# Optimization experiments

Measured on AMD Instinct MI355X. Metric: run time of the kernel, lower is better.

The kernel has to match this reference:

```python
import jax, jax.numpy as jnp
import numpy as np

# static config (matches init_kwargs)
B, CIN, L = 32, 128, 4096
COUT, K = 256, 5
PAD_SIZE = 2
INPUT_SCALE = 0.05
OUTPUT_SCALE = 0.1
INPUT_ZP = -3
OUTPUT_ZP = -128
QMIN, QMAX = -128, 127  # 8-bit signed range


def setup_inputs() -> dict:
    key = jax.random.key(0)
    k1, k2, k3, k4 = jax.random.split(key, 4)
    x = jax.random.normal(k1, (B, CIN, L), dtype=jnp.float32)
    weight = jax.random.randint(k2, (COUT, CIN, K), -127, 128, dtype=jnp.int32).astype(jnp.int8)
    # shifted quantized bias (int32), plausible magnitude
    bias = jax.random.randint(k3, (COUT,), -20000, 20000, dtype=jnp.int32)
    # per-output-channel weight scale
    weight_scale = jax.random.uniform(k4, (COUT,), dtype=jnp.float32, minval=1e-3, maxval=1e-2)
    return {"x": x, "weight": weight, "bias": bias, "weight_scale": weight_scale}


def reference(x, weight, bias, weight_scale):
    # --- linear_quantize (first_layer) ---
    xq = jnp.round(x / INPUT_SCALE) + INPUT_ZP
    xq = jnp.clip(xq, QMIN, QMAX).astype(jnp.int8)
    # --- ReplicationPad1d(pad_size) ---
    xq = jnp.pad(xq, ((0, 0), (0, 0), (PAD_SIZE, PAD_SIZE)), mode="edge")
    # --- int8 conv1d with int32 accumulation ---
    acc = jax.lax.conv_general_dilated(
        xq.astype(jnp.int32), weight.astype(jnp.int32),
        window_strides=(1,), padding=[(0, 0)],
        dimension_numbers=("NCH", "OIH", "NCH"))  # [B, COUT, Lout]
    acc = acc + bias[None, :, None]
    # --- per-channel requantization ---
    scale = (INPUT_SCALE * weight_scale / OUTPUT_SCALE)[None, :, None]
    out = acc.astype(jnp.float32) * scale + OUTPUT_ZP
    out = jnp.clip(jnp.round(out), QMIN, QMAX).astype(jnp.int8)
    return out
```

## Files before the change

### kernel.cpp

```cpp
#include <hip/hip_runtime.h>


#define B_    32
#define CIN   128
#define LEN   4096
#define COUT  256
#define KW    5
#define TROWS 136

#define WTF_BYTES (KW * 2 * 16 * 64 * 16)

typedef int          i32x4 __attribute__((ext_vector_type(4)));
typedef signed char  s8;

__device__ __forceinline__ s8 quant_i8(float xv) {
    float q = rintf(fmaf(xv, 20.0f, -3.0f));
    q = fminf(fmaxf(q, -128.0f), 127.0f);
    return (s8)(int)q;
}

__global__ __launch_bounds__(256) void wprep_kernel(
        const int* __restrict__ w, const int* __restrict__ bias,
        const float* __restrict__ wscale,
        s8* __restrict__ wtf, float* __restrict__ tbl)
{
    int o    = blockIdx.x * 256 + threadIdx.x;
    int lane = o & 63, frag = o >> 6;
    int k    = frag >> 5;
    int s    = (frag >> 4) & 1;
    int co   = ((frag & 15) << 4) + (lane & 15);
    int ci   = (s << 6) + ((lane >> 4) << 4);
    union { s8 c[16]; i32x4 v; } q;
    #pragma unroll
    for (int j = 0; j < 16; ++j)
        q.c[j] = (s8)w[co * (CIN * KW) + (ci + j) * KW + k];
    *(i32x4*)(wtf + (size_t)frag * 1024 + lane * 16) = q.v;

    if (blockIdx.x == 0) {
        int c = threadIdx.x;
        float sc = __fdiv_rn(__fmul_rn(0.05f, wscale[c]), 0.1f);
        tbl[c]       = sc;
        tbl[256 + c] = fmaf((float)bias[c], sc, -128.0f);
    }
}

__global__ __launch_bounds__(512, 4) void conv_fused(
        const float* __restrict__ x, const s8* __restrict__ wtf,
        const float* __restrict__ tbl, int* __restrict__ out)
{
    __shared__ __align__(16) s8 smem[TROWS * CIN];

    int orig  = (blockIdx.x & 7) * 128 + (blockIdx.x >> 3);
    int ltile = orig & 31;
    int b     = orig >> 5;
    int l0    = ltile << 7;
    int tid   = threadIdx.x;
    int wid   = tid >> 6, lane = tid & 63;
    int lr    = lane & 15, lh = lane >> 4;
    int cog   = (wid & 3) << 6;
    int wl    = (wid >> 2) << 6;

    const float* xb = x + (size_t)b * CIN * LEN;

    {
        const float* src = xb + (size_t)(wid << 4) * LEN;
        int gl0 = min(max(l0 - 4 + lane, 0), LEN - 1);
        int gl1 = min(max(l0 + 60 + lane, 0), LEN - 1);
        float v0[16], v1[16];
        #pragma unroll
        for (int j = 0; j < 16; ++j) {
            v0[j] = src[(size_t)j * LEN + gl0];
            v1[j] = src[(size_t)j * LEN + gl1];
        }
        union { s8 cc[16]; i32x4 v; } q0, q1;
        #pragma unroll
        for (int j = 0; j < 16; ++j) q0.cc[j] = quant_i8(v0[j]);
        #pragma unroll
        for (int j = 0; j < 16; ++j) q1.cc[j] = quant_i8(v1[j]);
        int row0 = lane, row1 = 64 + lane;
        *(i32x4*)(smem + (row0 << 7) + ((wid ^ (row0 & 7)) << 4)) = q0.v;
        *(i32x4*)(smem + (row1 << 7) + ((wid ^ (row1 & 7)) << 4)) = q1.v;
        if (lane < 8) {
            int row2 = 128 + lane;
            int gl2 = min(max(l0 + 124 + lane, 0), LEN - 1);
            union { s8 cc[16]; i32x4 v; } q2;
            #pragma unroll
            for (int j = 0; j < 16; ++j)
                q2.cc[j] = quant_i8(src[(size_t)j * LEN + gl2]);
            *(i32x4*)(smem + (row2 << 7) + ((wid ^ (row2 & 7)) << 4)) = q2.v;
        }
    }
    __syncthreads();

    i32x4 acc[4][4] = {};
    #pragma unroll
    for (int k = 0; k < KW; ++k) {
        #pragma unroll
        for (int s = 0; s < 2; ++s) {
            i32x4 af[4];
            #pragma unroll
            for (int ct = 0; ct < 4; ++ct)
                af[ct] = *(const i32x4*)(
                    wtf + (size_t)((k << 5) + (s << 4) + (cog >> 4) + ct) * 1024 + lane * 16);
            i32x4 bf[4];
            int chunk = (s << 2) + lh;
            #pragma unroll
            for (int lt = 0; lt < 4; ++lt) {
                int row = wl + (lt << 4) + lr + k + 2;
                bf[lt] = *(const i32x4*)(smem + (row << 7) + ((chunk ^ (row & 7)) << 4));
            }
            #pragma unroll
            for (int ct = 0; ct < 4; ++ct)
                #pragma unroll
                for (int lt = 0; lt < 4; ++lt)
                    acc[ct][lt] = __builtin_amdgcn_mfma_i32_16x16x64_i8(
                        bf[lt], af[ct], acc[ct][lt], 0, 0, 0);
        }
    }

    size_t outb = (size_t)b * COUT * LEN;
    #pragma unroll
    for (int ct = 0; ct < 4; ++ct) {
        int co = cog + (ct << 4) + lr;
        float scv = tbl[co];
        float off = tbl[256 + co];
        int* orow = out + outb + (size_t)co * LEN + l0 + wl + (lh << 2);
        #pragma unroll
        for (int lt = 0; lt < 4; ++lt) {
            i32x4 pk;
            #pragma unroll
            for (int r = 0; r < 4; ++r) {
                float o = rintf(fmaf((float)acc[ct][lt][r], scv, off));
                o = fminf(fmaxf(o, -128.0f), 127.0f);
                pk[r] = (int)o;
            }
            *(i32x4*)(orow + (lt << 4)) = pk;
        }
    }
}

extern "C" void kernel_launch(void* const* d_in, const int* in_sizes, int n_in,
                              void* d_out, int out_size, void* d_ws, size_t ws_size,
                              hipStream_t stream)
{
    const float* x    = (const float*)d_in[0];
    const int*   w    = (const int*)d_in[1];
    const int*   bias = (const int*)d_in[2];
    const float* wsc  = (const float*)d_in[3];
    int* out = (int*)d_out;

    s8*    wtf = (s8*)d_ws;
    float* tbl = (float*)((char*)d_ws + WTF_BYTES);

    wprep_kernel<<<dim3(40), dim3(256), 0, stream>>>(w, bias, wsc, wtf, tbl);
    conv_fused<<<dim3(1024), dim3(512), 0, stream>>>(x, wtf, tbl, out);
}
```

Before: 54.99 us.

## Halve conv tile length to 64 positions with 256-thread blocks

Each block now covers 64 output positions instead of 128, using 4 waves that each own 64 output channels, and the grid doubles to 2048 blocks. The input staging is reorganised so each wave loads two 16-channel groups, and the clamp on border indices is applied only for edge tiles. This gives more, smaller blocks and less shared memory per block, which should help occupancy and scheduling. The cost is a larger halo share per tile, so more redundant input loading and quantisation, and each weight fragment is reused across fewer positions.

```diff
diff --git a/kernel.cpp b/kernel.cpp
--- a/kernel.cpp
+++ b/kernel.cpp
@@ -6,7 +6,7 @@
 #define LEN   4096
 #define COUT  256
 #define KW    5
-#define TROWS 136
+#define TROWS 72
 
 #define WTF_BYTES (KW * 2 * 16 * 64 * 16)
 
@@ -44,50 +44,57 @@
     }
 }
 
-__global__ __launch_bounds__(512, 4) void conv_fused(
+__global__ __launch_bounds__(256, 4) void conv_fused(
         const float* __restrict__ x, const s8* __restrict__ wtf,
         const float* __restrict__ tbl, int* __restrict__ out)
 {
     __shared__ __align__(16) s8 smem[TROWS * CIN];
 
-    int orig  = (blockIdx.x & 7) * 128 + (blockIdx.x >> 3);
-    int ltile = orig & 31;
-    int b     = orig >> 5;
-    int l0    = ltile << 7;
+    int orig  = (blockIdx.x & 7) * 256 + (blockIdx.x >> 3);
+    int ltile = orig & 63;
+    int b     = orig >> 6;
+    int l0    = ltile << 6;
     int tid   = threadIdx.x;
     int wid   = tid >> 6, lane = tid & 63;
     int lr    = lane & 15, lh = lane >> 4;
-    int cog   = (wid & 3) << 6;
-    int wl    = (wid >> 2) << 6;
+    int cog   = wid << 6;
 
     const float* xb = x + (size_t)b * CIN * LEN;
 
     {
-        const float* src = xb + (size_t)(wid << 4) * LEN;
-        int gl0 = min(max(l0 - 4 + lane, 0), LEN - 1);
-        int gl1 = min(max(l0 + 60 + lane, 0), LEN - 1);
+        bool edge = (ltile == 0) | (ltile == 63);
+        const float* src0 = xb + (size_t)(wid << 4) * LEN;
+        const float* src1 = xb + (size_t)((wid + 4) << 4) * LEN;
+        int gl0 = l0 - 4 + lane;
+        if (edge) gl0 = min(max(gl0, 0), LEN - 1);
         float v0[16], v1[16];
         #pragma unroll
-        for (int j = 0; j < 16; ++j) {
-            v0[j] = src[(size_t)j * LEN + gl0];
-            v1[j] = src[(size_t)j * LEN + gl1];
-        }
+        for (int j = 0; j < 16; ++j) v0[j] = src0[(size_t)j * LEN + gl0];
+        #pragma unroll
+        for (int j = 0; j < 16; ++j) v1[j] = src1[(size_t)j * LEN + gl0];
         union { s8 cc[16]; i32x4 v; } q0, q1;
         #pragma unroll
         for (int j = 0; j < 16; ++j) q0.cc[j] = quant_i8(v0[j]);
         #pragma unroll
         for (int j = 0; j < 16; ++j) q1.cc[j] = quant_i8(v1[j]);
-        int row0 = lane, row1 = 64 + lane;
-        *(i32x4*)(smem + (row0 << 7) + ((wid ^ (row0 & 7)) << 4)) = q0.v;
-        *(i32x4*)(smem + (row1 << 7) + ((wid ^ (row1 & 7)) << 4)) = q1.v;
+        int row0 = lane;
+        int sw0  = (row0 & 7) << 4;
+        *(i32x4*)(smem + (row0 << 7) + (((wid) << 4) ^ sw0))     = q0.v;
+        *(i32x4*)(smem + (row0 << 7) + (((wid + 4) << 4) ^ sw0)) = q1.v;
         if (lane < 8) {
-            int row2 = 128 + lane;
-            int gl2 = min(max(l0 + 124 + lane, 0), LEN - 1);
-            union { s8 cc[16]; i32x4 v; } q2;
+            int row1 = 64 + lane;
+            int gl1 = l0 + 60 + lane;
+            if (edge) gl1 = min(gl1, LEN - 1);
+            union { s8 cc[16]; i32x4 v; } q2, q3;
             #pragma unroll
             for (int j = 0; j < 16; ++j)
-                q2.cc[j] = quant_i8(src[(size_t)j * LEN + gl2]);
-            *(i32x4*)(smem + (row2 << 7) + ((wid ^ (row2 & 7)) << 4)) = q2.v;
+                q2.cc[j] = quant_i8(src0[(size_t)j * LEN + gl1]);
+            #pragma unroll
+            for (int j = 0; j < 16; ++j)
+                q3.cc[j] = quant_i8(src1[(size_t)j * LEN + gl1]);
+            int sw1 = (row1 & 7) << 4;
+            *(i32x4*)(smem + (row1 << 7) + (((wid) << 4) ^ sw1))     = q2.v;
+            *(i32x4*)(smem + (row1 << 7) + (((wid + 4) << 4) ^ sw1)) = q3.v;
         }
     }
     __syncthreads();
@@ -106,7 +113,7 @@
             int chunk = (s << 2) + lh;
             #pragma unroll
             for (int lt = 0; lt < 4; ++lt) {
-                int row = wl + (lt << 4) + lr + k + 2;
+                int row = (lt << 4) + lr + k + 2;
                 bf[lt] = *(const i32x4*)(smem + (row << 7) + ((chunk ^ (row & 7)) << 4));
             }
             #pragma unroll
@@ -124,7 +131,7 @@
         int co = cog + (ct << 4) + lr;
         float scv = tbl[co];
         float off = tbl[256 + co];
-        int* orow = out + outb + (size_t)co * LEN + l0 + wl + (lh << 2);
+        int* orow = out + outb + (size_t)co * LEN + l0 + (lh << 2);
         #pragma unroll
         for (int lt = 0; lt < 4; ++lt) {
             i32x4 pk;
@@ -153,5 +160,5 @@
     float* tbl = (float*)((char*)d_ws + WTF_BYTES);
 
     wprep_kernel<<<dim3(40), dim3(256), 0, stream>>>(w, bias, wsc, wtf, tbl);
-    conv_fused<<<dim3(1024), dim3(512), 0, stream>>>(x, wtf, tbl, out);
+    conv_fused<<<dim3(2048), dim3(256), 0, stream>>>(x, wtf, tbl, out);
 }
```

After: 58.19 us. 5.8% more time.

## Warp-specialize conv into producer and MFMA waves with double-buffered LDS tiles

Applied to the files above, without the earlier changes.

Each block now covers four consecutive 128-wide L tiles instead of one, using 768 threads. Eight waves compute MFMAs while four producer waves load, quantize and stage the next tile into a second LDS buffer, with block-wide barriers between tiles. The aim is to overlap global x loads and quantization with matrix math and to amortize the per-block scale table loads. In exchange the grid shrinks to 256 blocks, which may underfill the GPU's compute units. The extra producer waves also add register and LDS pressure per block.

```diff
diff --git a/kernel.cpp b/kernel.cpp
--- a/kernel.cpp
+++ b/kernel.cpp
@@ -7,6 +7,8 @@
 #define COUT  256
 #define KW    5
 #define TROWS 136
+#define NT    4
+#define LDS_TILE 17408
 
 #define WTF_BYTES (KW * 2 * 16 * 64 * 16)
 
@@ -44,97 +46,127 @@
     }
 }
 
-__global__ __launch_bounds__(512, 4) void conv_fused(
+__device__ __forceinline__ void stage_chunk(
+        const float* __restrict__ xb, s8* __restrict__ buf,
+        int Lt, int c, int lane)
+{
+    const float* src = xb + (size_t)(c << 4) * LEN;
+    int gl0 = min(max(Lt - 4 + lane, 0), LEN - 1);
+    int gl1 = min(max(Lt + 60 + lane, 0), LEN - 1);
+    float v0[16], v1[16];
+    #pragma unroll
+    for (int j = 0; j < 16; ++j) {
+        v0[j] = src[(size_t)j * LEN + gl0];
+        v1[j] = src[(size_t)j * LEN + gl1];
+    }
+    union { s8 cc[16]; i32x4 v; } q0, q1;
+    #pragma unroll
+    for (int j = 0; j < 16; ++j) q0.cc[j] = quant_i8(v0[j]);
+    #pragma unroll
+    for (int j = 0; j < 16; ++j) q1.cc[j] = quant_i8(v1[j]);
+    int row0 = lane, row1 = 64 + lane;
+    *(i32x4*)(buf + (row0 << 7) + ((c ^ (row0 & 7)) << 4)) = q0.v;
+    *(i32x4*)(buf + (row1 << 7) + ((c ^ (row1 & 7)) << 4)) = q1.v;
+    if (lane < 8) {
+        int row2 = 128 + lane;
+        int gl2 = min(max(Lt + 124 + lane, 0), LEN - 1);
+        union { s8 cc[16]; i32x4 v; } q2;
+        #pragma unroll
+        for (int j = 0; j < 16; ++j)
+            q2.cc[j] = quant_i8(src[(size_t)j * LEN + gl2]);
+        *(i32x4*)(buf + (row2 << 7) + ((c ^ (row2 & 7)) << 4)) = q2.v;
+    }
+}
+
+__global__ __launch_bounds__(768, 3) void conv_fused(
         const float* __restrict__ x, const s8* __restrict__ wtf,
         const float* __restrict__ tbl, int* __restrict__ out)
 {
-    __shared__ __align__(16) s8 smem[TROWS * CIN];
+    __shared__ __align__(16) s8 smem[2 * LDS_TILE];
 
-    int orig  = (blockIdx.x & 7) * 128 + (blockIdx.x >> 3);
-    int ltile = orig & 31;
-    int b     = orig >> 5;
-    int l0    = ltile << 7;
-    int tid   = threadIdx.x;
-    int wid   = tid >> 6, lane = tid & 63;
-    int lr    = lane & 15, lh = lane >> 4;
-    int cog   = (wid & 3) << 6;
-    int wl    = (wid >> 2) << 6;
+    int orig = (blockIdx.x & 7) * 32 + (blockIdx.x >> 3);
+    int lseg = orig & 7;
+    int b    = orig >> 3;
+    int L0   = lseg << 9;
+    int tid  = threadIdx.x;
+    int wid  = tid >> 6, lane = tid & 63;
+    int lr   = lane & 15, lh = lane >> 4;
 
     const float* xb = x + (size_t)b * CIN * LEN;
 
-    {
-        const float* src = xb + (size_t)(wid << 4) * LEN;
-        int gl0 = min(max(l0 - 4 + lane, 0), LEN - 1);
-        int gl1 = min(max(l0 + 60 + lane, 0), LEN - 1);
-        float v0[16], v1[16];
-        #pragma unroll
-        for (int j = 0; j < 16; ++j) {
-            v0[j] = src[(size_t)j * LEN + gl0];
-            v1[j] = src[(size_t)j * LEN + gl1];
-        }
-        union { s8 cc[16]; i32x4 v; } q0, q1;
-        #pragma unroll
-        for (int j = 0; j < 16; ++j) q0.cc[j] = quant_i8(v0[j]);
-        #pragma unroll
-        for (int j = 0; j < 16; ++j) q1.cc[j] = quant_i8(v1[j]);
-        int row0 = lane, row1 = 64 + lane;
-        *(i32x4*)(smem + (row0 << 7) + ((wid ^ (row0 & 7)) << 4)) = q0.v;
-        *(i32x4*)(smem + (row1 << 7) + ((wid ^ (row1 & 7)) << 4)) = q1.v;
-        if (lane < 8) {
-            int row2 = 128 + lane;
-            int gl2 = min(max(l0 + 124 + lane, 0), LEN - 1);
-            union { s8 cc[16]; i32x4 v; } q2;
-            #pragma unroll
-            for (int j = 0; j < 16; ++j)
-                q2.cc[j] = quant_i8(src[(size_t)j * LEN + gl2]);
-            *(i32x4*)(smem + (row2 << 7) + ((wid ^ (row2 & 7)) << 4)) = q2.v;
-        }
-    }
+    if (wid < 8)
+        stage_chunk(xb, smem, L0, wid, lane);
     __syncthreads();
 
-    i32x4 acc[4][4] = {};
-    #pragma unroll
-    for (int k = 0; k < KW; ++k) {
+    size_t outb = (size_t)b * COUT * LEN;
+
+    if (wid < 8) {
+        int cog = (wid & 3) << 6;
+        int wl  = (wid >> 2) << 6;
+        float scv[4], offv[4];
         #pragma unroll
-        for (int s = 0; s < 2; ++s) {
-            i32x4 af[4];
+        for (int ct = 0; ct < 4; ++ct) {
+            scv[ct]  = tbl[cog + (ct << 4) + lr];
+            offv[ct] = tbl[256 + cog + (ct << 4) + lr];
+        }
+        for (int t = 0; t < NT; ++t) {
+            const s8* buf = smem + (t & 1) * LDS_TILE;
+            int l0 = L0 + (t << 7);
+
+            i32x4 acc[4][4] = {};
             #pragma unroll
-            for (int ct = 0; ct < 4; ++ct)
-                af[ct] = *(const i32x4*)(
-                    wtf + (size_t)((k << 5) + (s << 4) + (cog >> 4) + ct) * 1024 + lane * 16);
-            i32x4 bf[4];
-            int chunk = (s << 2) + lh;
+            for (int k = 0; k < KW; ++k) {
+                #pragma unroll
+                for (int s = 0; s < 2; ++s) {
+                    i32x4 af[4];
+                    #pragma unroll
+                    for (int ct = 0; ct < 4; ++ct)
+                        af[ct] = *(const i32x4*)(
+                            wtf + (size_t)((k << 5) + (s << 4) + (cog >> 4) + ct) * 1024 + lane * 16);
+                    i32x4 bf[4];
+                    int chunk = (s << 2) + lh;
+                    #pragma unroll
+                    for (int lt = 0; lt < 4; ++lt) {
+                        int row = wl + (lt << 4) + lr + k + 2;
+                        bf[lt] = *(const i32x4*)(buf + (row << 7) + ((chunk ^ (row & 7)) << 4));
+                    }
+                    #pragma unroll
+                    for (int ct = 0; ct < 4; ++ct)
+                        #pragma unroll
+                        for (int lt = 0; lt < 4; ++lt)
+                            acc[ct][lt] = __builtin_amdgcn_mfma_i32_16x16x64_i8(
+                                bf[lt], af[ct], acc[ct][lt], 0, 0, 0);
+                }
+            }
+
             #pragma unroll
-            for (int lt = 0; lt < 4; ++lt) {
-                int row = wl + (lt << 4) + lr + k + 2;
-                bf[lt] = *(const i32x4*)(smem + (row << 7) + ((chunk ^ (row & 7)) << 4));
+            for (int ct = 0; ct < 4; ++ct) {
+                int co = cog + (ct << 4) + lr;
+                int* orow = out + outb + (size_t)co * LEN + l0 + wl + (lh << 2);
+                #pragma unroll
+                for (int lt = 0; lt < 4; ++lt) {
+                    i32x4 pk;
+                    #pragma unroll
+                    for (int r = 0; r < 4; ++r) {
+                        float o = rintf(fmaf((float)acc[ct][lt][r], scv[ct], offv[ct]));
+                        o = fminf(fmaxf(o, -128.0f), 127.0f);
+                        pk[r] = (int)o;
+                    }
+                    *(i32x4*)(orow + (lt << 4)) = pk;
+                }
             }
-            #pragma unroll
-            for (int ct = 0; ct < 4; ++ct)
-                #pragma unroll
-                for (int lt = 0; lt < 4; ++lt)
-                    acc[ct][lt] = __builtin_amdgcn_mfma_i32_16x16x64_i8(
-                        bf[lt], af[ct], acc[ct][lt], 0, 0, 0);
+            __syncthreads();
         }
-    }
-
-    size_t outb = (size_t)b * COUT * LEN;
-    #pragma unroll
-    for (int ct = 0; ct < 4; ++ct) {
-        int co = cog + (ct << 4) + lr;
-        float scv = tbl[co];
-        float off = tbl[256 + co];
-        int* orow = out + outb + (size_t)co * LEN + l0 + wl + (lh << 2);
-        #pragma unroll
-        for (int lt = 0; lt < 4; ++lt) {
-            i32x4 pk;
-            #pragma unroll
-            for (int r = 0; r < 4; ++r) {
-                float o = rintf(fmaf((float)acc[ct][lt][r], scv, off));
-                o = fminf(fmaxf(o, -128.0f), 127.0f);
-                pk[r] = (int)o;
+    } else {
+        int pw = wid - 8;
+        for (int t = 0; t < NT; ++t) {
+            if (t + 1 < NT) {
+                s8* nbuf = smem + ((t + 1) & 1) * LDS_TILE;
+                int Ln = L0 + ((t + 1) << 7);
+                stage_chunk(xb, nbuf, Ln, pw, lane);
+                stage_chunk(xb, nbuf, Ln, pw + 4, lane);
             }
-            *(i32x4*)(orow + (lt << 4)) = pk;
+            __syncthreads();
         }
     }
 }
@@ -153,5 +185,5 @@
     float* tbl = (float*)((char*)d_ws + WTF_BYTES);
 
     wprep_kernel<<<dim3(40), dim3(256), 0, stream>>>(w, bias, wsc, wtf, tbl);
-    conv_fused<<<dim3(1024), dim3(512), 0, stream>>>(x, wtf, tbl, out);
+    conv_fused<<<dim3(256), dim3(768), 0, stream>>>(x, wtf, tbl, out);
 }
```

Result: slower. 101.9 us (+85.3%).
